# Kernel optimization log

Measured on AMD Instinct MI355X. Metric: run time of the kernel, lower is better.

The kernel has to match this reference:

```python
import jax, jax.numpy as jnp
import numpy as np
from jax import lax

B, C, H, W = 32, 1, 1024, 1024
P = 100            # points per image (all exactly 1.0 in target)
LOCAL = 33         # local_size
OFF = LOCAL // 2   # 16
CS = 2 * OFF       # crop size: [y-off:y+off) -> 32
C1 = 0.01 ** 2
C2 = 0.03 ** 2


def gaussian_window(ws, sigma=1.5):
    x = jnp.arange(ws, dtype=jnp.float32) - ws // 2
    g = jnp.exp(-(x * x) / (2.0 * sigma * sigma))
    g = g / g.sum()
    return jnp.outer(g, g)  # [ws, ws]


def setup_inputs() -> dict:
    key = jax.random.key(0)
    k1, k2, k3, k4 = jax.random.split(key, 4)
    output = jax.random.uniform(k1, (B, C, H, W), jnp.float32)
    target = jax.random.uniform(k2, (B, C, H, W), jnp.float32)
    # interior points so every local crop is a full 32x32 (no boundary clipping)
    ys = jax.random.randint(k3, (B, P), OFF, H - OFF)
    xs = jax.random.randint(k4, (B, P), OFF, W - OFF)
    b_idx = jnp.arange(B)[:, None]
    target = target.at[b_idx, 0, ys, xs].set(1.0)  # points where target == 1.0
    points = jnp.stack([ys, xs], axis=-1).astype(jnp.int32)  # [B, P, 2]
    return {"output": output, "target": target, "points": points}


def _crops(imgs, points):
    # imgs: [B, C, H, W]; points: [B, P, 2] -> [B, P, C, CS, CS]
    def crop_img(img, pts):
        def one(pt):
            return lax.dynamic_slice(img, (0, pt[0] - OFF, pt[1] - OFF), (C, CS, CS))
        return jax.vmap(one)(pts)
    return jax.vmap(crop_img)(imgs, points)


def _dwconv(x, w):
    # depthwise conv, same padding (ws odd); x: [N, C, s, s], w: [C, 1, ws, ws]
    return lax.conv_general_dilated(
        x, w, window_strides=(1, 1), padding=[(OFF, OFF), (OFF, OFF)],
        dimension_numbers=("NCHW", "OIHW", "NCHW"), feature_group_count=C)


def _issim(output, target, points):
    win = jnp.broadcast_to(gaussian_window(LOCAL), (C, 1, LOCAL, LOCAL))
    t = _crops(target, points).reshape(B * P, C, CS, CS)
    o = _crops(output, points).reshape(B * P, C, CS, CS)
    mu1 = _dwconv(t, win)
    mu2 = _dwconv(o, win)
    mu1_sq, mu2_sq, mu1_mu2 = mu1 * mu1, mu2 * mu2, mu1 * mu2
    sigma1_sq = _dwconv(t * t, win) - mu1_sq
    sigma2_sq = _dwconv(o * o, win) - mu2_sq
    sigma12 = _dwconv(t * o, win) - mu1_mu2
    ssim_map = ((2 * mu1_mu2 + C1) * (2 * sigma12 + C2)) / (
        (mu1_sq + mu2_sq + C1) * (sigma1_sq + sigma2_sq + C2))
    per_crop = (1.0 - ssim_map).sum(axis=(1, 2, 3))        # ssim_loss(..., reduction='sum')
    per_image = per_crop.reshape(B, P).sum(axis=1) / P     # divide by n_points
    return per_image.mean()                                # reduction='mean'


def reference(output, target, points):
    return _issim(output, target, points)
```

## Files before the change

### kernel.cpp

```cpp
#include <hip/hip_runtime.h>
#include <math.h>

#define NB    32
#define NP    100
#define IMH   1024
#define IMW   1024
#define CS    32
#define OFFS  16
#define NTAP  33
#define C1c   0.0001f
#define C2c   0.0009f

struct GWin { float g[NTAP]; };

__global__ __launch_bounds__(256) void issim_crops(
    const float* __restrict__ outp,
    const float* __restrict__ tgt,
    const int*   __restrict__ pts,
    float* __restrict__ partial,
    GWin gw)
{
    __shared__ float tp[CS][64];
    __shared__ float op[CS][64];
    __shared__ float ht[CS][CS], ho[CS][CS], htt[CS][CS], hoo[CS][CS], hto[CS][CS];

    const int bp = blockIdx.x;
    const int b  = bp / NP;
    const int y  = pts[bp * 2 + 0];
    const int x  = pts[bp * 2 + 1];
    const float* tb = tgt  + (size_t)b * IMH * IMW;
    const float* ob = outp + (size_t)b * IMH * IMW;

    const int tid = threadIdx.x;

#pragma unroll
    for (int k = 0; k < 8; ++k) {
        int idx = tid + k * 256;
        int r = idx >> 6, c = idx & 63;
        float tv = 0.f, ov = 0.f;
        if (c >= OFFS && c < OFFS + CS) {
            int gr = y - OFFS + r;
            int gc = x - OFFS + (c - OFFS);
            size_t a = (size_t)gr * IMW + gc;
            tv = tb[a];
            ov = ob[a];
        }
        tp[r][c] = tv;
        op[r][c] = ov;
    }
    __syncthreads();

#pragma unroll
    for (int k = 0; k < 4; ++k) {
        int f = tid + k * 256;
        int r = f >> 5, j = f & 31;
        float at = 0.f, ao = 0.f, att = 0.f, aoo = 0.f, ato = 0.f;
#pragma unroll
        for (int kj = 0; kj < NTAP; ++kj) {
            float w  = gw.g[kj];
            float tv = tp[r][j + kj];
            float ov = op[r][j + kj];
            at  += w * tv;
            ao  += w * ov;
            att += w * tv * tv;
            aoo += w * ov * ov;
            ato += w * tv * ov;
        }
        ht[r][j]  = at;
        ho[r][j]  = ao;
        htt[r][j] = att;
        hoo[r][j] = aoo;
        hto[r][j] = ato;
    }
    __syncthreads();

    float lsum = 0.f;
#pragma unroll
    for (int k = 0; k < 4; ++k) {
        int f = tid + k * 256;
        int i = f >> 5, j = f & 31;
        int klo = OFFS - i;       if (klo < 0)    klo = 0;
        int khi = OFFS + CS - i;  if (khi > NTAP) khi = NTAP;
        float at = 0.f, ao = 0.f, att = 0.f, aoo = 0.f, ato = 0.f;
        for (int ki = klo; ki < khi; ++ki) {
            int r = i - OFFS + ki;
            float w = gw.g[ki];
            at  += w * ht[r][j];
            ao  += w * ho[r][j];
            att += w * htt[r][j];
            aoo += w * hoo[r][j];
            ato += w * hto[r][j];
        }
        float mu1  = at, mu2 = ao;
        float mu1s = mu1 * mu1, mu2s = mu2 * mu2, mu12 = mu1 * mu2;
        float s1   = att - mu1s;
        float s2   = aoo - mu2s;
        float s12  = ato - mu12;
        float num  = (2.f * mu12 + C1c) * (2.f * s12 + C2c);
        float den  = (mu1s + mu2s + C1c) * (s1 + s2 + C2c);
        lsum += 1.f - num / den;
    }

#pragma unroll
    for (int d = 32; d > 0; d >>= 1) lsum += __shfl_down(lsum, d, 64);
    __shared__ float wsum[4];
    int wid = tid >> 6, lane = tid & 63;
    if (lane == 0) wsum[wid] = lsum;
    __syncthreads();
    if (tid == 0) partial[bp] = wsum[0] + wsum[1] + wsum[2] + wsum[3];
}

__global__ __launch_bounds__(256) void issim_reduce(
    const float* __restrict__ partial, float* __restrict__ out)
{
    const int tid = threadIdx.x;
    float s = 0.f;
    for (int i = tid; i < NB * NP; i += 256) s += partial[i];
#pragma unroll
    for (int d = 32; d > 0; d >>= 1) s += __shfl_down(s, d, 64);
    __shared__ float wsum[4];
    int wid = tid >> 6, lane = tid & 63;
    if (lane == 0) wsum[wid] = s;
    __syncthreads();
    if (tid == 0) out[0] = (wsum[0] + wsum[1] + wsum[2] + wsum[3]) / (float)(NB * NP);
}

extern "C" void kernel_launch(void* const* d_in, const int* in_sizes, int n_in,
                              void* d_out, int out_size, void* d_ws, size_t ws_size,
                              hipStream_t stream) {
    const float* outp = (const float*)d_in[0];
    const float* tgt  = (const float*)d_in[1];
    const int*   pts  = (const int*)d_in[2];
    float* partial = (float*)d_ws;
    float* out     = (float*)d_out;

    GWin gw;
    {
        double raw[NTAP], s = 0.0;
        for (int i = 0; i < NTAP; ++i) {
            double xv = (double)i - (double)(NTAP / 2);
            raw[i] = exp(-(xv * xv) / (2.0 * 1.5 * 1.5));
            s += raw[i];
        }
        for (int i = 0; i < NTAP; ++i) gw.g[i] = (float)(raw[i] / s);
    }

    issim_crops<<<NB * NP, 256, 0, stream>>>(outp, tgt, pts, partial, gw);
    issim_reduce<<<1, 256, 0, stream>>>(partial, out);
}
```

Before: 290.3 us.

## Register-block separable SSIM convolutions and pack intermediates into aliased shared memory

Each thread now computes 4 adjacent outputs in both the horizontal and vertical Gaussian passes, reusing each loaded input value across 4 taps from registers. This cuts LDS reads per output and precomputes the products tt/oo/to once per loaded element. Shared memory is packed into one aliased buffer with a padded stride of 65 to avoid bank conflicts. The horizontal intermediates are stored as float4 plus one float, which lowers LDS footprint and may raise occupancy. The cost is more registers from 20 accumulators per thread, and the vertical pass now iterates over out-of-range rows with predication instead of clamping the loop bounds.

```diff
diff --git a/kernel.cpp b/kernel.cpp
--- a/kernel.cpp
+++ b/kernel.cpp
@@ -10,8 +10,11 @@
 #define NTAP  33
 #define C1c   0.0001f
 #define C2c   0.0009f
+#define PSTR  65
 
 struct GWin { float g[NTAP]; };
+
+#define SMEM_BYTES 20480
 
 __global__ __launch_bounds__(256) void issim_crops(
     const float* __restrict__ outp,
@@ -20,9 +23,12 @@
     float* __restrict__ partial,
     GWin gw)
 {
-    __shared__ float tp[CS][64];
-    __shared__ float op[CS][64];
-    __shared__ float ht[CS][CS], ho[CS][CS], htt[CS][CS], hoo[CS][CS], hto[CS][CS];
+    __shared__ __align__(16) char smem[SMEM_BYTES];
+    __shared__ float wsum[4];
+    float  (*tp)[PSTR] = (float (*)[PSTR])smem;
+    float  (*op)[PSTR] = (float (*)[PSTR])(smem + CS * PSTR * 4);
+    float4 (*vh4)[CS]  = (float4 (*)[CS])smem;
+    float  (*vh1)[CS]  = (float (*)[CS])(smem + 16384);
 
     const int bp = blockIdx.x;
     const int b  = bp / NP;
@@ -30,80 +36,103 @@
     const int x  = pts[bp * 2 + 1];
     const float* tb = tgt  + (size_t)b * IMH * IMW;
     const float* ob = outp + (size_t)b * IMH * IMW;
-
     const int tid = threadIdx.x;
 
 #pragma unroll
-    for (int k = 0; k < 8; ++k) {
-        int idx = tid + k * 256;
-        int r = idx >> 6, c = idx & 63;
-        float tv = 0.f, ov = 0.f;
-        if (c >= OFFS && c < OFFS + CS) {
-            int gr = y - OFFS + r;
-            int gc = x - OFFS + (c - OFFS);
-            size_t a = (size_t)gr * IMW + gc;
-            tv = tb[a];
-            ov = ob[a];
+    for (int kk = 0; kk < 4; ++kk) {
+        int idx = tid + kk * 256;
+        int r = idx >> 5, c = idx & 31;
+        size_t a = (size_t)(y - OFFS + r) * IMW + (x - OFFS + c);
+        tp[r][c + OFFS] = tb[a];
+        op[r][c + OFFS] = ob[a];
+        int cz = (c < OFFS) ? c : (c + 32);
+        tp[r][cz] = 0.f;
+        op[r][cz] = 0.f;
+    }
+    __syncthreads();
+
+    const int hr = tid >> 3;
+    const int j0 = (tid & 7) * 4;
+    float at[4]  = {0.f, 0.f, 0.f, 0.f};
+    float ao[4]  = {0.f, 0.f, 0.f, 0.f};
+    float att[4] = {0.f, 0.f, 0.f, 0.f};
+    float aoo[4] = {0.f, 0.f, 0.f, 0.f};
+    float ato[4] = {0.f, 0.f, 0.f, 0.f};
+#pragma unroll
+    for (int k = 0; k < 36; ++k) {
+        float tv = tp[hr][j0 + k];
+        float ov = op[hr][j0 + k];
+        float tt = tv * tv, oo = ov * ov, to = tv * ov;
+#pragma unroll
+        for (int m = 0; m < 4; ++m) {
+            int ki = k - m;
+            if (ki >= 0 && ki < NTAP) {
+                float w = gw.g[ki];
+                at[m]  += w * tv;
+                ao[m]  += w * ov;
+                att[m] += w * tt;
+                aoo[m] += w * oo;
+                ato[m] += w * to;
+            }
         }
-        tp[r][c] = tv;
-        op[r][c] = ov;
     }
     __syncthreads();
 
 #pragma unroll
-    for (int k = 0; k < 4; ++k) {
-        int f = tid + k * 256;
-        int r = f >> 5, j = f & 31;
-        float at = 0.f, ao = 0.f, att = 0.f, aoo = 0.f, ato = 0.f;
-#pragma unroll
-        for (int kj = 0; kj < NTAP; ++kj) {
-            float w  = gw.g[kj];
-            float tv = tp[r][j + kj];
-            float ov = op[r][j + kj];
-            at  += w * tv;
-            ao  += w * ov;
-            att += w * tv * tv;
-            aoo += w * ov * ov;
-            ato += w * tv * ov;
-        }
-        ht[r][j]  = at;
-        ho[r][j]  = ao;
-        htt[r][j] = att;
-        hoo[r][j] = aoo;
-        hto[r][j] = ato;
+    for (int m = 0; m < 4; ++m) {
+        vh4[hr][j0 + m] = make_float4(at[m], ao[m], att[m], aoo[m]);
+        vh1[hr][j0 + m] = ato[m];
     }
     __syncthreads();
 
+    const int vj = tid & 31;
+    const int i0 = (tid >> 5) * 4;
+    float vt[4]  = {0.f, 0.f, 0.f, 0.f};
+    float vo[4]  = {0.f, 0.f, 0.f, 0.f};
+    float vtt[4] = {0.f, 0.f, 0.f, 0.f};
+    float voo[4] = {0.f, 0.f, 0.f, 0.f};
+    float vto[4] = {0.f, 0.f, 0.f, 0.f};
+#pragma unroll
+    for (int k = 0; k < 36; ++k) {
+        int row = i0 + k - OFFS;
+        bool rv = (row >= 0) && (row < CS);
+        int rc = row & 31;
+        float4 h4 = vh4[rc][vj];
+        float  h1 = vh1[rc][vj];
+        float a0 = rv ? h4.x : 0.f;
+        float a1 = rv ? h4.y : 0.f;
+        float a2 = rv ? h4.z : 0.f;
+        float a3 = rv ? h4.w : 0.f;
+        float a4 = rv ? h1   : 0.f;
+#pragma unroll
+        for (int m = 0; m < 4; ++m) {
+            int ki = k - m;
+            if (ki >= 0 && ki < NTAP) {
+                float w = gw.g[ki];
+                vt[m]  += w * a0;
+                vo[m]  += w * a1;
+                vtt[m] += w * a2;
+                voo[m] += w * a3;
+                vto[m] += w * a4;
+            }
+        }
+    }
+
     float lsum = 0.f;
 #pragma unroll
-    for (int k = 0; k < 4; ++k) {
-        int f = tid + k * 256;
-        int i = f >> 5, j = f & 31;
-        int klo = OFFS - i;       if (klo < 0)    klo = 0;
-        int khi = OFFS + CS - i;  if (khi > NTAP) khi = NTAP;
-        float at = 0.f, ao = 0.f, att = 0.f, aoo = 0.f, ato = 0.f;
-        for (int ki = klo; ki < khi; ++ki) {
-            int r = i - OFFS + ki;
-            float w = gw.g[ki];
-            at  += w * ht[r][j];
-            ao  += w * ho[r][j];
-            att += w * htt[r][j];
-            aoo += w * hoo[r][j];
-            ato += w * hto[r][j];
-        }
-        float mu1  = at, mu2 = ao;
+    for (int m = 0; m < 4; ++m) {
+        float mu1 = vt[m], mu2 = vo[m];
         float mu1s = mu1 * mu1, mu2s = mu2 * mu2, mu12 = mu1 * mu2;
-        float s1   = att - mu1s;
-        float s2   = aoo - mu2s;
-        float s12  = ato - mu12;
-        float num  = (2.f * mu12 + C1c) * (2.f * s12 + C2c);
-        float den  = (mu1s + mu2s + C1c) * (s1 + s2 + C2c);
+        float s1  = vtt[m] - mu1s;
+        float s2  = voo[m] - mu2s;
+        float s12 = vto[m] - mu12;
+        float num = (2.f * mu12 + C1c) * (2.f * s12 + C2c);
+        float den = (mu1s + mu2s + C1c) * (s1 + s2 + C2c);
         lsum += 1.f - num / den;
     }
 
 #pragma unroll
     for (int d = 32; d > 0; d >>= 1) lsum += __shfl_down(lsum, d, 64);
-    __shared__ float wsum[4];
     int wid = tid >> 6, lane = tid & 63;
     if (lane == 0) wsum[wid] = lsum;
     __syncthreads();
```

Result: faster. 255.6 us (-12.0%).
